# Kernel optimization log

Hardware: AMD Instinct MI355X
Metric: run time of the kernel (lower is better)

## Reference

```python
import jax, jax.numpy as jnp
import numpy as np

N_NODES = 100000
N_EDGES = 1600000
N_FEAT = 128
H_CH = 64
N_GRAPHS = 4096
N_LAY = 3


def _gcn_conv(x, W, bias, src, dst, dinv):
    # GCNConv with self-loops: out = D^{-1/2}(A+I)D^{-1/2} (x W) + bias
    h = x @ W  # [N, out]
    coef = (dinv[src] * dinv[dst])[:, None]  # [E, 1]
    agg = jax.ops.segment_sum(h[src] * coef, dst, num_segments=N_NODES)
    agg = agg + h * (dinv * dinv)[:, None]  # self-loop term
    return agg + bias


def setup_inputs() -> dict:
    key = jax.random.key(0)
    ks = jax.random.split(key, 12)
    x = jax.random.normal(ks[0], (N_NODES, N_FEAT), dtype=jnp.float32)
    e_idx = jax.random.randint(ks[1], (2, N_EDGES), 0, N_NODES, dtype=jnp.int32)
    b = jnp.sort(jax.random.randint(ks[2], (N_NODES,), 0, N_GRAPHS, dtype=jnp.int32))
    s = 0.05
    w0 = jax.random.normal(ks[3], (N_FEAT, H_CH), dtype=jnp.float32) * s
    b0 = jax.random.normal(ks[4], (H_CH,), dtype=jnp.float32) * s
    convW = jax.random.normal(ks[5], (N_LAY - 1, H_CH, H_CH), dtype=jnp.float32) * s
    convB = jax.random.normal(ks[6], (N_LAY - 1, H_CH), dtype=jnp.float32) * s
    skipW = jax.random.normal(ks[7], (N_LAY - 1, H_CH, H_CH), dtype=jnp.float32) * s
    skipB = jax.random.normal(ks[8], (N_LAY - 1, H_CH), dtype=jnp.float32) * s
    lin1W = jax.random.normal(ks[9], (H_CH, H_CH // 2), dtype=jnp.float32) * s
    lin1b = jnp.zeros((H_CH // 2,), dtype=jnp.float32)
    lin2W = jax.random.normal(ks[10], (H_CH // 2, 1), dtype=jnp.float32) * s
    lin2b = jnp.zeros((1,), dtype=jnp.float32)
    return {"x": x, "e_idx": e_idx, "b": b, "w0": w0, "b0": b0,
            "convW": convW, "convB": convB, "skipW": skipW, "skipB": skipB,
            "lin1W": lin1W, "lin1b": lin1b, "lin2W": lin2W, "lin2b": lin2b}


def reference(x, e_idx, b, w0, b0, convW, convB, skipW, skipB, lin1W, lin1b, lin2W, lin2b):
    src, dst = e_idx[0], e_idx[1]
    # degree (with self-loop) computed on destination nodes, as in PyG GCNConv
    deg = jax.ops.segment_sum(jnp.ones((N_EDGES,), x.dtype), dst, num_segments=N_NODES) + 1.0
    dinv = jax.lax.rsqrt(deg)

    h = jax.nn.relu(_gcn_conv(x, w0, b0, src, dst, dinv))  # dropout: eval mode identity
    for i in range(N_LAY - 1):
        h_n = jax.nn.relu(_gcn_conv(h, convW[i], convB[i], src, dst, dinv))
        h_s = h @ skipW[i] + skipB[i]
        h = h_n + h_s

    # global mean pool over graph ids
    sums = jax.ops.segment_sum(h, b, num_segments=N_GRAPHS)
    cnts = jax.ops.segment_sum(jnp.ones((N_NODES,), x.dtype), b, num_segments=N_GRAPHS)
    pooled = sums / jnp.maximum(cnts, 1.0)[:, None]  # [G, H]

    out = jax.nn.relu(pooled @ lin1W + lin1b)
    return out @ lin2W + lin2b  # [G, 1]
```

## Files before the change

### kernel.cpp

```cpp
#include <hip/hip_runtime.h>
#include <hip/hip_fp16.h>

#define NN 100000
#define NE 1600000
#define NF 128
#define H  64
#define NG 4096

#define NBK 512
#define BKN 196
#define CAP 4096
#define NBLK_BIN 256
#define CHUNK ((NE + NBLK_BIN - 1) / NBLK_BIN)

typedef unsigned long long u64;
typedef unsigned int u32;

__device__ inline u32 packh2(float x, float y) {
  __half2 h = __floats2half2_rn(x, y);
  return *reinterpret_cast<u32*>(&h);
}
__device__ inline float2 unpackh2(u32 u) {
  __half2 h = *reinterpret_cast<__half2*>(&u);
  return __half22float2(h);
}

__global__ __launch_bounds__(256) void k_bin(const int* __restrict__ src,
                                             const int* __restrict__ dst,
                                             int* __restrict__ bcur,
                                             u32* __restrict__ ebuf) {
  __shared__ int d_s[CHUNK];
  __shared__ int bcnt[NBK], bpos[NBK];
  const int e0 = blockIdx.x * CHUNK;
  const int e1 = min(e0 + CHUNK, NE);
  for (int i = threadIdx.x; i < NBK; i += 256) bcnt[i] = 0;
  __syncthreads();
  for (int e = e0 + threadIdx.x; e < e1; e += 256) {
    const int d = dst[e];
    d_s[e - e0] = d;
    atomicAdd(&bcnt[d / BKN], 1);
  }
  __syncthreads();
  for (int i = threadIdx.x; i < NBK; i += 256) {
    const int c = bcnt[i];
    if (c) bpos[i] = i * CAP + atomicAdd(&bcur[i], c);
  }
  __syncthreads();
  for (int e = e0 + threadIdx.x; e < e1; e += 256) {
    const int d = d_s[e - e0];
    const int bk = d / BKN;
    const int pos = atomicAdd(&bpos[bk], 1);
    ebuf[pos] = ((u32)(d - bk * BKN) << 17) | (u32)src[e];
  }
}

__global__ __launch_bounds__(256) void k_csr(const int* __restrict__ bcur,
                                             const u32* __restrict__ ebuf,
                                             int* __restrict__ row_ptr,
                                             int* __restrict__ cnt,
                                             float* __restrict__ dinv,
                                             int* __restrict__ csr_src) {
  __shared__ u32 eb_s[CAP];
  __shared__ int deg[256], sc[256], cur[256];
  const int bk = blockIdx.x;
  const int nlo = bk * BKN;
  if (nlo >= NN) return;
  const int nloc = min(BKN, NN - nlo);
  const int cntE = bcur[bk];
  const int t = threadIdx.x;
  for (int e = t; e < cntE; e += 256) eb_s[e] = ebuf[(size_t)bk * CAP + e];
  deg[t] = 0;
  __syncthreads();
  for (int e = t; e < cntE; e += 256) atomicAdd(&deg[eb_s[e] >> 17], 1);
  __syncthreads();
  sc[t] = deg[t];
  __syncthreads();
  for (int off = 1; off < 256; off <<= 1) {
    const int add = (t >= off) ? sc[t - off] : 0;
    __syncthreads();
    sc[t] += add;
    __syncthreads();
  }
  const int excl = bk * CAP + sc[t] - deg[t];
  if (t < nloc) {
    row_ptr[nlo + t] = excl;
    cnt[nlo + t] = deg[t];
    dinv[nlo + t] = 1.0f / sqrtf((float)deg[t] + 1.0f);
  }
  cur[t] = excl;
  __syncthreads();
  for (int oct = 0; oct < 8; ++oct) {
    for (int e = t; e < cntE; e += 256) {
      const u32 ent = eb_s[e];
      const int s = (int)(ent & 0x1ffffu);
      if (((s >> 14) & 7) == oct) {
        const int pos = atomicAdd(&cur[ent >> 17], 1);
        csr_src[pos] = s << 4;
      }
    }
    __syncthreads();
  }
  for (int e = cntE + t; e < min(cntE + 64, CAP); e += 256)
    csr_src[bk * CAP + e] = 0;
}

__global__ __launch_bounds__(256) void k_obin(const int* __restrict__ cnt,
                                              int* __restrict__ gcur) {
  __shared__ int lh[64];
  const int t = threadIdx.x;
  if (t < 64) lh[t] = 0;
  __syncthreads();
  const int n = blockIdx.x * 256 + t;
  if (n < NN) atomicAdd(&lh[min(cnt[n], 63)], 1);
  __syncthreads();
  if (t < 64 && lh[t]) atomicAdd(&gcur[t], lh[t]);
}

__global__ __launch_bounds__(64) void k_oscan(int* __restrict__ gcur) {
  __shared__ int sh[64];
  const int t = threadIdx.x;
  const int v = gcur[t];
  sh[t] = v;
  __syncthreads();
  for (int off = 1; off < 64; off <<= 1) {
    const int a = (t >= off) ? sh[t - off] : 0;
    __syncthreads();
    sh[t] += a;
    __syncthreads();
  }
  gcur[t] = sh[t] - v;
}

__global__ __launch_bounds__(256) void k_oscat(const int* __restrict__ cnt,
                                               int* __restrict__ gcur,
                                               int* __restrict__ order) {
  __shared__ int lh[64], lo[64];
  const int t = threadIdx.x;
  if (t < 64) lh[t] = 0;
  __syncthreads();
  const int n = blockIdx.x * 256 + t;
  int bin = 0, loc = 0;
  if (n < NN) {
    bin = min(cnt[n], 63);
    loc = atomicAdd(&lh[bin], 1);
  }
  __syncthreads();
  if (t < 64 && lh[t]) lo[t] = atomicAdd(&gcur[t], lh[t]);
  __syncthreads();
  if (n < NN) order[lo[bin] + loc] = n;
}

#define TSTR 388
template <int CI, bool SK>
__global__ __launch_bounds__(256) void k_gemm(const float* __restrict__ in,
                                              const float* __restrict__ W,
                                              const float* __restrict__ Ws,
                                              const float* __restrict__ bs,
                                              const float* __restrict__ dinv,
                                              u32* __restrict__ out16,
                                              float* __restrict__ outS) {
  __shared__ float wt[CI * 64];
  __shared__ float wsl[SK ? 64 * 64 : 1];
  __shared__ float tin[8 * TSTR];
  for (int i = threadIdx.x; i < CI * 64; i += 256) wt[i] = W[i];
  if (SK)
    for (int i = threadIdx.x; i < 64 * 64; i += 256) wsl[i] = Ws[i];

  const int row0 = blockIdx.x * 256;
  const int rg = threadIdx.x >> 3;
  const int cg = threadIdx.x & 7;
  float acc[8][8];
  float sacc[SK ? 8 : 1][SK ? 8 : 1];
#pragma unroll
  for (int i = 0; i < 8; ++i)
#pragma unroll
    for (int j = 0; j < 8; ++j) acc[i][j] = 0.0f;
  if (SK) {
#pragma unroll
    for (int i = 0; i < 8; ++i)
#pragma unroll
      for (int j = 0; j < 8; ++j) sacc[i][j] = bs[cg * 8 + j];
  }

  const int kk = (threadIdx.x & 1) * 4;
  const int rr = threadIdx.x >> 1;
  for (int k0 = 0; k0 < CI; k0 += 8) {
    __syncthreads();
#pragma unroll
    for (int s = 0; s < 2; ++s) {
      const int r = s * 128 + rr;
      const int rowc = min(row0 + r, NN - 1);
      const float4 v = *(const float4*)(in + (size_t)rowc * CI + k0 + kk);
      const int base = (r >> 3) * 12 + (r & 7);
      tin[(kk + 0) * TSTR + base] = v.x;
      tin[(kk + 1) * TSTR + base] = v.y;
      tin[(kk + 2) * TSTR + base] = v.z;
      tin[(kk + 3) * TSTR + base] = v.w;
    }
    __syncthreads();
#pragma unroll
    for (int k = 0; k < 8; ++k) {
      const float4 a0 = *(const float4*)&tin[k * TSTR + rg * 12];
      const float4 a1 = *(const float4*)&tin[k * TSTR + rg * 12 + 4];
      const float af[8] = {a0.x, a0.y, a0.z, a0.w, a1.x, a1.y, a1.z, a1.w};
      const float4 b0 = *(const float4*)&wt[(k0 + k) * 64 + cg * 8];
      const float4 b1 = *(const float4*)&wt[(k0 + k) * 64 + cg * 8 + 4];
      const float bf[8] = {b0.x, b0.y, b0.z, b0.w, b1.x, b1.y, b1.z, b1.w};
#pragma unroll
      for (int i = 0; i < 8; ++i)
#pragma unroll
        for (int j = 0; j < 8; ++j) acc[i][j] = fmaf(af[i], bf[j], acc[i][j]);
      if (SK) {
        const float4 c0 = *(const float4*)&wsl[(k0 + k) * 64 + cg * 8];
        const float4 c1 = *(const float4*)&wsl[(k0 + k) * 64 + cg * 8 + 4];
        const float cf[8] = {c0.x, c0.y, c0.z, c0.w, c1.x, c1.y, c1.z, c1.w};
#pragma unroll
        for (int i = 0; i < 8; ++i)
#pragma unroll
          for (int j = 0; j < 8; ++j) sacc[i][j] = fmaf(af[i], cf[j], sacc[i][j]);
      }
    }
  }
#pragma unroll
  for (int i = 0; i < 8; ++i) {
    const int row = row0 + rg * 8 + i;
    if (row < NN) {
      const float dv = dinv[row];
      u32 o[4];
#pragma unroll
      for (int j = 0; j < 4; ++j)
        o[j] = packh2(acc[i][2 * j] * dv, acc[i][2 * j + 1] * dv);
      *(uint4*)&out16[(size_t)row * 32 + cg * 4] =
          make_uint4(o[0], o[1], o[2], o[3]);
      if (SK) {
        float* sp = outS + (size_t)row * 64 + cg * 8;
        *(float4*)(sp) = make_float4(sacc[i][0], sacc[i][1], sacc[i][2], sacc[i][3]);
        *(float4*)(sp + 4) = make_float4(sacc[i][4], sacc[i][5], sacc[i][6], sacc[i][7]);
      }
    }
  }
}

template <bool ADD_S>
__global__ __launch_bounds__(256) void k_agg(const u32* __restrict__ hw16,
                                             const float* __restrict__ hs,
                                             const int* __restrict__ csr_src,
                                             const int* __restrict__ row_ptr,
                                             const int* __restrict__ cnt,
                                             const float* __restrict__ dinv,
                                             const float* __restrict__ bias,
                                             const int* __restrict__ order,
                                             float* __restrict__ h) {
  const int lane = threadIdx.x & 63;
  const int grp  = lane >> 4;
  const int cl   = lane & 15;
  const int wv   = threadIdx.x >> 6;
  const int slot = (blockIdx.x * 4 + wv) * 4 + grp;
  const int n = order[slot];
  const int beg = row_ptr[n];
  const int deg = cnt[n];
  const int d1 = max(deg, __shfl_xor(deg, 16));
  const int dmax = max(d1, __shfl_xor(d1, 32));
  const u64* hw64 = (const u64*)hw16;
  float4 acc = make_float4(0.f, 0.f, 0.f, 0.f);
  int i = 0;

#define GSTEP(NK)                                                             \
  {                                                                           \
    int p[NK];                                                                \
    uint2 uv[NK];                                                             \
    _Pragma("unroll") for (int k = 0; k < NK; ++k)                            \
        p[k] = __builtin_nontemporal_load(&csr_src[beg + i + k]);             \
    _Pragma("unroll") for (int k = 0; k < NK; ++k)                            \
        uv[k] = *(const uint2*)&hw64[(size_t)(p[k] + cl)];                    \
    _Pragma("unroll") for (int k = 0; k < NK; ++k) {                          \
      const float m = ((i + k) < deg) ? 1.0f : 0.0f;                          \
      const float2 f0 = unpackh2(uv[k].x);                                    \
      const float2 f1 = unpackh2(uv[k].y);                                    \
      acc.x = fmaf(f0.x, m, acc.x);                                           \
      acc.y = fmaf(f0.y, m, acc.y);                                           \
      acc.z = fmaf(f1.x, m, acc.z);                                           \
      acc.w = fmaf(f1.y, m, acc.w);                                           \
    }                                                                         \
    i += NK;                                                                  \
  }

  while (i + 8 <= dmax) GSTEP(8)
  if (i + 4 <= dmax) GSTEP(4)
  if (i + 2 <= dmax) GSTEP(2)
  if (i < dmax) GSTEP(1)
#undef GSTEP

  const uint2 sv = *(const uint2*)&hw64[(size_t)n * 16 + cl];
  const float2 s0 = unpackh2(sv.x);
  const float2 s1 = unpackh2(sv.y);
  const float dv = dinv[n];
  const float4 brc = *(const float4*)&bias[cl * 4];
  float4 r;
  r.x = fmaxf((acc.x + s0.x) * dv + brc.x, 0.0f);
  r.y = fmaxf((acc.y + s0.y) * dv + brc.y, 0.0f);
  r.z = fmaxf((acc.z + s1.x) * dv + brc.z, 0.0f);
  r.w = fmaxf((acc.w + s1.y) * dv + brc.w, 0.0f);
  if (ADD_S) {
    const float4 s = *(const float4*)&hs[(size_t)n * 64 + cl * 4];
    r.x += s.x; r.y += s.y; r.z += s.z; r.w += s.w;
  }
  *(float4*)&h[(size_t)n * 64 + cl * 4] = r;
}

__global__ __launch_bounds__(256) void k_pool(const float* __restrict__ h,
                                              const int* __restrict__ b,
                                              float* __restrict__ pool,
                                              float* __restrict__ cnt) {
  const int col = threadIdx.x & 63;
  const int wv  = threadIdx.x >> 6;
  const int node0 = (blockIdx.x * 4 + wv) * 64;
  if (node0 >= NN) return;
  const int node1 = min(node0 + 64, NN);
  int gcur = b[node0];
  float acc = 0.f;
  float run = 0.f;
  for (int n = node0; n < node1; ++n) {
    const int g = b[n];
    if (g != gcur) {
      atomicAdd(&pool[(size_t)gcur * 64 + col], acc);
      if (col == 0) atomicAdd(&cnt[gcur], run);
      gcur = g; acc = 0.f; run = 0.f;
    }
    acc += h[(size_t)n * 64 + col];
    run += 1.f;
  }
  atomicAdd(&pool[(size_t)gcur * 64 + col], acc);
  if (col == 0) atomicAdd(&cnt[gcur], run);
}

__global__ __launch_bounds__(64) void k_head(const float* __restrict__ pool,
                                             const float* __restrict__ cnt,
                                             const float* __restrict__ lin1W,
                                             const float* __restrict__ lin1b,
                                             const float* __restrict__ lin2W,
                                             const float* __restrict__ lin2b,
                                             float* __restrict__ out) {
  const int g = blockIdx.x;
  const int lane = threadIdx.x;
  const float c = fmaxf(cnt[g], 1.0f);
  float r = 0.f;
  if (lane < 32) {
    float s = lin1b[lane];
    const float* p = pool + (size_t)g * 64;
#pragma unroll 8
    for (int ci = 0; ci < 64; ++ci) s = fmaf(p[ci] / c, lin1W[ci * 32 + lane], s);
    r = fmaxf(s, 0.0f) * lin2W[lane];
  }
  for (int off = 32; off > 0; off >>= 1) r += __shfl_down(r, off, 64);
  if (lane == 0) out[g] = r + lin2b[0];
}

extern "C" void kernel_launch(void* const* d_in, const int* in_sizes, int n_in,
                              void* d_out, int out_size, void* d_ws, size_t ws_size,
                              hipStream_t stream) {
  const float* x     = (const float*)d_in[0];
  const int*   src   = (const int*)d_in[1];
  const int*   dst   = ((const int*)d_in[1]) + NE;
  const int*   b     = (const int*)d_in[2];
  const float* w0    = (const float*)d_in[3];
  const float* b0    = (const float*)d_in[4];
  const float* convW = (const float*)d_in[5];
  const float* convB = (const float*)d_in[6];
  const float* skipW = (const float*)d_in[7];
  const float* skipB = (const float*)d_in[8];
  const float* lin1W = (const float*)d_in[9];
  const float* lin1b = (const float*)d_in[10];
  const float* lin2W = (const float*)d_in[11];
  const float* lin2b = (const float*)d_in[12];
  float* out = (float*)d_out;

  char* w = (char*)d_ws;
  const size_t NPAD = 102400;
  int*   cnt     = (int*)w;                  w += NPAD * 4;
  float* dinv    = (float*)w;                w += NPAD * 4;
  int*   row_ptr = (int*)w;                  w += NPAD * 4;
  int*   order   = (int*)w;                  w += NPAD * 4;
  int*   bcur    = (int*)w;                  w += 1024 * 4;
  int*   gcur    = (int*)w;                  w += 1024 * 4;
  int*   csr_src = (int*)w;                  w += (size_t)NBK * CAP * 4 + 4096;
  char*  big     = w;                        w += (size_t)NN * 32 * 4;
  float* hA      = (float*)w;                w += (size_t)NN * 64 * 4;
  float* hS      = (float*)w;                w += (size_t)NN * 64 * 4;
  float* pool    = (float*)w;                w += (size_t)NG * 64 * 4;
  float* pcnt    = (float*)w;                w += (size_t)NG * 4;
  u32* ebuf = (u32*)big;
  u32* hw16 = (u32*)big;

  hipMemsetAsync(bcur, 0, NBK * sizeof(int), stream);
  hipMemsetAsync(gcur, 0, 64 * sizeof(int), stream);
  k_bin<<<NBLK_BIN, 256, 0, stream>>>(src, dst, bcur, ebuf);
  k_csr<<<NBK, 256, 0, stream>>>(bcur, ebuf, row_ptr, cnt, dinv, csr_src);
  const int OB = (NN + 255) / 256;
  k_obin<<<OB, 256, 0, stream>>>(cnt, gcur);
  k_oscan<<<1, 64, 0, stream>>>(gcur);
  k_oscat<<<OB, 256, 0, stream>>>(cnt, gcur, order);

  const int GT = (NN + 255) / 256;

  k_gemm<NF, false><<<GT, 256, 0, stream>>>(x, w0, nullptr, nullptr, dinv,
                                            hw16, nullptr);
  k_agg<false><<<6250, 256, 0, stream>>>(hw16, nullptr, csr_src, row_ptr, cnt,
                                         dinv, b0, order, hA);
  for (int i = 0; i < 2; ++i) {
    k_gemm<H, true><<<GT, 256, 0, stream>>>(hA, convW + (size_t)i * H * H,
                                            skipW + (size_t)i * H * H,
                                            skipB + (size_t)i * H, dinv, hw16, hS);
    k_agg<true><<<6250, 256, 0, stream>>>(hw16, hS, csr_src, row_ptr, cnt,
                                          dinv, convB + (size_t)i * H, order, hA);
  }

  hipMemsetAsync(pool, 0, ((size_t)NG * 64 + NG) * sizeof(float), stream);
  k_pool<<<(NN / 256) + 1, 256, 0, stream>>>(hA, b, pool, pcnt);
  k_head<<<NG, 64, 0, stream>>>(pool, pcnt, lin1W, lin1b, lin2W, lin2b, out);
}
```

Baseline: 323.3 us.

## Widen aggregation gathers to 16-byte loads with 8 nodes per wavefront and double-buffered indices

Each node's 64 fp16 features are now gathered by 8 lanes using 128-bit loads instead of 16 lanes using 64-bit loads, so each wavefront handles 8 nodes and the grid is halved. The CSR source index is rescaled to match the new stride. Neighbor index loads are double-buffered in groups of 8 so index fetches overlap the feature gathers. The aim is fewer, wider memory transactions and better latency hiding, at the cost of more registers per lane and padding of the degree loop up to a multiple of 8, which relies on the zero-filled tail of csr_src.

```diff
diff --git a/kernel.cpp b/kernel.cpp
--- a/kernel.cpp
+++ b/kernel.cpp
@@ -95,7 +95,7 @@
       const int s = (int)(ent & 0x1ffffu);
       if (((s >> 14) & 7) == oct) {
         const int pos = atomicAdd(&cur[ent >> 17], 1);
-        csr_src[pos] = s << 4;
+        csr_src[pos] = s << 3;
       }
     }
     __syncthreads();
@@ -252,60 +252,85 @@
                                              const int* __restrict__ order,
                                              float* __restrict__ h) {
   const int lane = threadIdx.x & 63;
-  const int grp  = lane >> 4;
-  const int cl   = lane & 15;
+  const int grp  = lane >> 3;
+  const int cl   = lane & 7;
   const int wv   = threadIdx.x >> 6;
-  const int slot = (blockIdx.x * 4 + wv) * 4 + grp;
+  const int slot = (blockIdx.x * 4 + wv) * 8 + grp;
   const int n = order[slot];
   const int beg = row_ptr[n];
   const int deg = cnt[n];
-  const int d1 = max(deg, __shfl_xor(deg, 16));
+  int d1 = max(deg, __shfl_xor(deg, 8));
+  d1 = max(d1, __shfl_xor(d1, 16));
   const int dmax = max(d1, __shfl_xor(d1, 32));
-  const u64* hw64 = (const u64*)hw16;
-  float4 acc = make_float4(0.f, 0.f, 0.f, 0.f);
-  int i = 0;
-
-#define GSTEP(NK)                                                             \
+  const uint4* hw128 = (const uint4*)hw16;
+  float acc[8];
+#pragma unroll
+  for (int j = 0; j < 8; ++j) acc[j] = 0.0f;
+
+#define LOADI(BUF, BASE)                                                      \
+  _Pragma("unroll") for (int k = 0; k < 8; ++k)                               \
+      BUF[k] = __builtin_nontemporal_load(&csr_src[beg + (BASE) + k]);
+
+#define CONSUME(BUF, BASE)                                                    \
   {                                                                           \
-    int p[NK];                                                                \
-    uint2 uv[NK];                                                             \
-    _Pragma("unroll") for (int k = 0; k < NK; ++k)                            \
-        p[k] = __builtin_nontemporal_load(&csr_src[beg + i + k]);             \
-    _Pragma("unroll") for (int k = 0; k < NK; ++k)                            \
-        uv[k] = *(const uint2*)&hw64[(size_t)(p[k] + cl)];                    \
-    _Pragma("unroll") for (int k = 0; k < NK; ++k) {                          \
-      const float m = ((i + k) < deg) ? 1.0f : 0.0f;                          \
+    uint4 uv[8];                                                              \
+    _Pragma("unroll") for (int k = 0; k < 8; ++k)                             \
+        uv[k] = hw128[(size_t)(BUF[k] + cl)];                                 \
+    _Pragma("unroll") for (int k = 0; k < 8; ++k) {                           \
+      const float m = (((BASE) + k) < deg) ? 1.0f : 0.0f;                     \
       const float2 f0 = unpackh2(uv[k].x);                                    \
       const float2 f1 = unpackh2(uv[k].y);                                    \
-      acc.x = fmaf(f0.x, m, acc.x);                                           \
-      acc.y = fmaf(f0.y, m, acc.y);                                           \
-      acc.z = fmaf(f1.x, m, acc.z);                                           \
-      acc.w = fmaf(f1.y, m, acc.w);                                           \
+      const float2 f2 = unpackh2(uv[k].z);                                    \
+      const float2 f3 = unpackh2(uv[k].w);                                    \
+      acc[0] = fmaf(f0.x, m, acc[0]);                                         \
+      acc[1] = fmaf(f0.y, m, acc[1]);                                         \
+      acc[2] = fmaf(f1.x, m, acc[2]);                                         \
+      acc[3] = fmaf(f1.y, m, acc[3]);                                         \
+      acc[4] = fmaf(f2.x, m, acc[4]);                                         \
+      acc[5] = fmaf(f2.y, m, acc[5]);                                         \
+      acc[6] = fmaf(f3.x, m, acc[6]);                                         \
+      acc[7] = fmaf(f3.y, m, acc[7]);                                         \
     }                                                                         \
-    i += NK;                                                                  \
-  }
-
-  while (i + 8 <= dmax) GSTEP(8)
-  if (i + 4 <= dmax) GSTEP(4)
-  if (i + 2 <= dmax) GSTEP(2)
-  if (i < dmax) GSTEP(1)
-#undef GSTEP
-
-  const uint2 sv = *(const uint2*)&hw64[(size_t)n * 16 + cl];
+  }
+
+  const int dm8 = ((dmax + 7) >> 3) << 3;
+  if (dm8 > 0) {
+    int idxA[8], idxB[8];
+    LOADI(idxA, 0)
+    int base = 0;
+    for (; base + 8 < dm8; base += 16) {
+      LOADI(idxB, base + 8)
+      CONSUME(idxA, base)
+      if (base + 16 < dm8) LOADI(idxA, base + 16)
+      CONSUME(idxB, base + 8)
+    }
+    if (base < dm8) CONSUME(idxA, base)
+  }
+#undef LOADI
+#undef CONSUME
+
+  const uint4 sv = hw128[(size_t)n * 8 + cl];
   const float2 s0 = unpackh2(sv.x);
   const float2 s1 = unpackh2(sv.y);
+  const float2 s2 = unpackh2(sv.z);
+  const float2 s3 = unpackh2(sv.w);
+  const float sf[8] = {s0.x, s0.y, s1.x, s1.y, s2.x, s2.y, s3.x, s3.y};
   const float dv = dinv[n];
-  const float4 brc = *(const float4*)&bias[cl * 4];
-  float4 r;
-  r.x = fmaxf((acc.x + s0.x) * dv + brc.x, 0.0f);
-  r.y = fmaxf((acc.y + s0.y) * dv + brc.y, 0.0f);
-  r.z = fmaxf((acc.z + s1.x) * dv + brc.z, 0.0f);
-  r.w = fmaxf((acc.w + s1.y) * dv + brc.w, 0.0f);
+  const float4 b0 = *(const float4*)&bias[cl * 8];
+  const float4 b1 = *(const float4*)&bias[cl * 8 + 4];
+  const float bf[8] = {b0.x, b0.y, b0.z, b0.w, b1.x, b1.y, b1.z, b1.w};
+  float r[8];
+#pragma unroll
+  for (int j = 0; j < 8; ++j)
+    r[j] = fmaxf((acc[j] + sf[j]) * dv + bf[j], 0.0f);
   if (ADD_S) {
-    const float4 s = *(const float4*)&hs[(size_t)n * 64 + cl * 4];
-    r.x += s.x; r.y += s.y; r.z += s.z; r.w += s.w;
-  }
-  *(float4*)&h[(size_t)n * 64 + cl * 4] = r;
+    const float4 h0 = *(const float4*)&hs[(size_t)n * 64 + cl * 8];
+    const float4 h1 = *(const float4*)&hs[(size_t)n * 64 + cl * 8 + 4];
+    r[0] += h0.x; r[1] += h0.y; r[2] += h0.z; r[3] += h0.w;
+    r[4] += h1.x; r[5] += h1.y; r[6] += h1.z; r[7] += h1.w;
+  }
+  *(float4*)&h[(size_t)n * 64 + cl * 8] = make_float4(r[0], r[1], r[2], r[3]);
+  *(float4*)&h[(size_t)n * 64 + cl * 8 + 4] = make_float4(r[4], r[5], r[6], r[7]);
 }
 
 __global__ __launch_bounds__(256) void k_pool(const float* __restrict__ h,
@@ -405,13 +430,13 @@
 
   k_gemm<NF, false><<<GT, 256, 0, stream>>>(x, w0, nullptr, nullptr, dinv,
                                             hw16, nullptr);
-  k_agg<false><<<6250, 256, 0, stream>>>(hw16, nullptr, csr_src, row_ptr, cnt,
+  k_agg<false><<<3125, 256, 0, stream>>>(hw16, nullptr, csr_src, row_ptr, cnt,
                                          dinv, b0, order, hA);
   for (int i = 0; i < 2; ++i) {
     k_gemm<H, true><<<GT, 256, 0, stream>>>(hA, convW + (size_t)i * H * H,
                                             skipW + (size_t)i * H * H,
                                             skipB + (size_t)i * H, dinv, hw16, hS);
-    k_agg<true><<<6250, 256, 0, stream>>>(hw16, hS, csr_src, row_ptr, cnt,
+    k_agg<true><<<3125, 256, 0, stream>>>(hw16, hS, csr_src, row_ptr, cnt,
                                           dinv, convB + (size_t)i * H, order, hA);
   }
 
```

New measurement: 328.8 us. No clear change (+1.7%).

## Rewrite dense GEMM with fp16 dot2 instructions and whole-tile LDS staging

Applied to the files above, without the earlier changes.

The dense transform kernels now convert inputs and weights to packed half precision and accumulate with the fdot2 intrinsic (two multiply-adds per instruction) in fp32. The whole K dimension for a 128-row tile is staged into LDS once with an XOR swizzle, instead of looping over 8-wide K slices with barriers. Each block now covers 128 rows, so the grid doubles. This cuts FMA instruction count and synchronisation, but rounding inputs and weights to fp16 adds error to the GEMM results.

```diff
diff --git a/kernel.cpp b/kernel.cpp
--- a/kernel.cpp
+++ b/kernel.cpp
@@ -15,6 +15,7 @@
 
 typedef unsigned long long u64;
 typedef unsigned int u32;
+typedef __attribute__((ext_vector_type(2))) _Float16 h2;
 
 __device__ inline u32 packh2(float x, float y) {
   __half2 h = __floats2half2_rn(x, y);
@@ -24,6 +25,16 @@
   __half2 h = *reinterpret_cast<__half2*>(&u);
   return __half22float2(h);
 }
+
+#if __has_builtin(__builtin_amdgcn_fdot2)
+__device__ inline float dot2(h2 a, h2 b, float c) {
+  return __builtin_amdgcn_fdot2(a, b, c, false);
+}
+#else
+__device__ inline float dot2(h2 a, h2 b, float c) {
+  return fmaf((float)a.x, (float)b.x, fmaf((float)a.y, (float)b.y, c));
+}
+#endif
 
 __global__ __launch_bounds__(256) void k_bin(const int* __restrict__ src,
                                              const int* __restrict__ dst,
@@ -150,7 +161,7 @@
   if (n < NN) order[lo[bin] + loc] = n;
 }
 
-#define TSTR 388
+#define TXOR(row) ((((row) >> 3) & 3) << 2)
 template <int CI, bool SK>
 __global__ __launch_bounds__(256) void k_gemm(const float* __restrict__ in,
                                               const float* __restrict__ W,
@@ -159,71 +170,89 @@
                                               const float* __restrict__ dinv,
                                               u32* __restrict__ out16,
                                               float* __restrict__ outS) {
-  __shared__ float wt[CI * 64];
-  __shared__ float wsl[SK ? 64 * 64 : 1];
-  __shared__ float tin[8 * TSTR];
-  for (int i = threadIdx.x; i < CI * 64; i += 256) wt[i] = W[i];
-  if (SK)
-    for (int i = threadIdx.x; i < 64 * 64; i += 256) wsl[i] = Ws[i];
-
-  const int row0 = blockIdx.x * 256;
+  constexpr int KP = CI / 2;
+  constexpr int RS = KP + 4;
+  constexpr int WS = KP + 4;
+  __shared__ h2 tin2[128 * RS];
+  __shared__ h2 wt2[64 * WS];
+  __shared__ h2 wsl2[SK ? 64 * WS : 1];
+  union U2 { uint2 u; h2 h[2]; };
+  union U4 { uint4 u; h2 h[4]; };
+
+  const int row0 = blockIdx.x * 128;
+  for (int i = threadIdx.x; i < 64 * KP; i += 256) {
+    const int c = i & 63;
+    const int kp = i >> 6;
+    wt2[c * WS + kp] = h2{(_Float16)W[(2 * kp) * 64 + c],
+                          (_Float16)W[(2 * kp + 1) * 64 + c]};
+    if (SK)
+      wsl2[c * WS + kp] = h2{(_Float16)Ws[(2 * kp) * 64 + c],
+                             (_Float16)Ws[(2 * kp + 1) * 64 + c]};
+  }
+  for (int s = 0; s < (128 * CI) / 1024; ++s) {
+    const int idx = (s * 256 + threadIdx.x) * 4;
+    const int r = idx / CI;
+    const int k = idx % CI;
+    const int rowc = min(row0 + r, NN - 1);
+    const float4 v = *(const float4*)(in + (size_t)rowc * CI + k);
+    U2 a;
+    a.h[0] = h2{(_Float16)v.x, (_Float16)v.y};
+    a.h[1] = h2{(_Float16)v.z, (_Float16)v.w};
+    const int kp = (k >> 1) ^ TXOR(r);
+    *(uint2*)&tin2[r * RS + kp] = a.u;
+  }
+  __syncthreads();
+
   const int rg = threadIdx.x >> 3;
   const int cg = threadIdx.x & 7;
-  float acc[8][8];
-  float sacc[SK ? 8 : 1][SK ? 8 : 1];
-#pragma unroll
-  for (int i = 0; i < 8; ++i)
+  float acc[4][8];
+  float sacc[SK ? 4 : 1][8];
+#pragma unroll
+  for (int i = 0; i < 4; ++i)
 #pragma unroll
     for (int j = 0; j < 8; ++j) acc[i][j] = 0.0f;
   if (SK) {
 #pragma unroll
-    for (int i = 0; i < 8; ++i)
+    for (int i = 0; i < 4; ++i)
 #pragma unroll
       for (int j = 0; j < 8; ++j) sacc[i][j] = bs[cg * 8 + j];
   }
 
-  const int kk = (threadIdx.x & 1) * 4;
-  const int rr = threadIdx.x >> 1;
-  for (int k0 = 0; k0 < CI; k0 += 8) {
-    __syncthreads();
-#pragma unroll
-    for (int s = 0; s < 2; ++s) {
-      const int r = s * 128 + rr;
-      const int rowc = min(row0 + r, NN - 1);
-      const float4 v = *(const float4*)(in + (size_t)rowc * CI + k0 + kk);
-      const int base = (r >> 3) * 12 + (r & 7);
-      tin[(kk + 0) * TSTR + base] = v.x;
-      tin[(kk + 1) * TSTR + base] = v.y;
-      tin[(kk + 2) * TSTR + base] = v.z;
-      tin[(kk + 3) * TSTR + base] = v.w;
+  const int tx = TXOR(rg * 4);
+#pragma unroll 2
+  for (int kq = 0; kq < KP / 4; ++kq) {
+    U4 A[4], B[8];
+#pragma unroll
+    for (int r = 0; r < 4; ++r)
+      A[r].u = *(const uint4*)&tin2[(rg * 4 + r) * RS + ((kq * 4) ^ tx)];
+#pragma unroll
+    for (int c = 0; c < 8; ++c)
+      B[c].u = *(const uint4*)&wt2[(cg * 8 + c) * WS + kq * 4];
+#pragma unroll
+    for (int r = 0; r < 4; ++r)
+#pragma unroll
+      for (int c = 0; c < 8; ++c)
+#pragma unroll
+        for (int q = 0; q < 4; ++q)
+          acc[r][c] = dot2(A[r].h[q], B[c].h[q], acc[r][c]);
+    if (SK) {
+      U4 C[8];
+#pragma unroll
+      for (int c = 0; c < 8; ++c)
+        C[c].u = *(const uint4*)&wsl2[(cg * 8 + c) * WS + kq * 4];
+#pragma unroll
+      for (int r = 0; r < 4; ++r)
+#pragma unroll
+        for (int c = 0; c < 8; ++c)
+#pragma unroll
+          for (int q = 0; q < 4; ++q)
+            sacc[r][c] = dot2(A[r].h[q], C[c].h[q], sacc[r][c]);
     }
-    __syncthreads();
-#pragma unroll
-    for (int k = 0; k < 8; ++k) {
-      const float4 a0 = *(const float4*)&tin[k * TSTR + rg * 12];
-      const float4 a1 = *(const float4*)&tin[k * TSTR + rg * 12 + 4];
-      const float af[8] = {a0.x, a0.y, a0.z, a0.w, a1.x, a1.y, a1.z, a1.w};
-      const float4 b0 = *(const float4*)&wt[(k0 + k) * 64 + cg * 8];
-      const float4 b1 = *(const float4*)&wt[(k0 + k) * 64 + cg * 8 + 4];
-      const float bf[8] = {b0.x, b0.y, b0.z, b0.w, b1.x, b1.y, b1.z, b1.w};
-#pragma unroll
-      for (int i = 0; i < 8; ++i)
-#pragma unroll
-        for (int j = 0; j < 8; ++j) acc[i][j] = fmaf(af[i], bf[j], acc[i][j]);
-      if (SK) {
-        const float4 c0 = *(const float4*)&wsl[(k0 + k) * 64 + cg * 8];
-        const float4 c1 = *(const float4*)&wsl[(k0 + k) * 64 + cg * 8 + 4];
-        const float cf[8] = {c0.x, c0.y, c0.z, c0.w, c1.x, c1.y, c1.z, c1.w};
-#pragma unroll
-        for (int i = 0; i < 8; ++i)
-#pragma unroll
-          for (int j = 0; j < 8; ++j) sacc[i][j] = fmaf(af[i], cf[j], sacc[i][j]);
-      }
-    }
-  }
-#pragma unroll
-  for (int i = 0; i < 8; ++i) {
-    const int row = row0 + rg * 8 + i;
+  }
+
+#pragma unroll
+  for (int i = 0; i < 4; ++i) {
+    const int row = row0 + rg * 4 + i;
     if (row < NN) {
       const float dv = dinv[row];
       u32 o[4];
@@ -401,7 +430,7 @@
   k_oscan<<<1, 64, 0, stream>>>(gcur);
   k_oscat<<<OB, 256, 0, stream>>>(cnt, gcur, order);
 
-  const int GT = (NN + 255) / 256;
+  const int GT = (NN + 127) / 128;
 
   k_gemm<NF, false><<<GT, 256, 0, stream>>>(x, w0, nullptr, nullptr, dinv,
                                             hw16, nullptr);
```

Result: faster. 316.3 us (-2.2%).
